# Performance work log

Hardware: AMD Instinct MI355X
Metric: run time of the kernel (lower is better)

Reference implementation:

```python
import jax, jax.numpy as jnp
import numpy as np

TEMPERATURE = 0.2
NUMBER_CLASSES = 1000
LOSS_SCALE = 0.001

N, F = 8192, 256
M = 20000
DEPTH = 4


def setup_inputs() -> dict:
    key = jax.random.key(0)
    k1, k2, k3, k4 = jax.random.split(key, 4)
    gt_labels = jax.random.randint(k1, (N,), 0, NUMBER_CLASSES, dtype=jnp.int32)
    box_features = jax.random.normal(k2, (N, F), dtype=jnp.float32)
    memory = jax.random.normal(k3, (M, F), dtype=jnp.float32)
    trace_idx = jax.random.randint(k4, (NUMBER_CLASSES, DEPTH), 0, M, dtype=jnp.int32)
    return {"gt_labels": gt_labels, "box_features": box_features,
            "memory": memory, "trace_idx": trace_idx}


def reference(gt_labels, box_features, memory, trace_idx):
    # logits[i, j] = dot(f_i, m_j) / T  (the nested python loops fused into one GEMM)
    logits = jnp.einsum('nf,mf->nm', box_features, memory) / TEMPERATURE  # [N, M]
    # fenmu = sum_j exp(logits)  ->  log(fenmu) = logsumexp
    lse = jax.nn.logsumexp(logits, axis=-1)  # [N]
    # gather the trace entries for each item's label: [N, DEPTH]
    traces = trace_idx[gt_labels]  # [N, DEPTH]
    sel = jnp.take_along_axis(logits, traces, axis=1)  # [N, DEPTH]
    depth_w = jnp.arange(DEPTH, dtype=logits.dtype)  # gj = depth
    sum_gj = depth_w.sum()  # sum of layer weights (0+1+2+3)
    # per item: -sum_d gj * log(sim_d / fenmu) / sum_gj
    per_item = -jnp.sum((sel - lse[:, None]) * depth_w, axis=-1) / sum_gj  # [N]
    # background filter: items with label == number_classes contribute nothing
    fg = (gt_labels != NUMBER_CLASSES)
    loss = jnp.sum(jnp.where(fg, per_item, 0.0)) * LOSS_SCALE
    return loss
```

## Files before the change

kernel.cpp:

```cpp
#include <hip/hip_runtime.h>
#include <hip/hip_bf16.h>
#include <stdint.h>

#define NROWS 8192
#define FDIM 256
#define MCOLS 20000
#define NT32 625
#define MSPLIT 16
#define NCLS 1000
#define LOG2E 1.44269504088896f
#define LN2   0.69314718055994f


typedef short short8 __attribute__((ext_vector_type(8)));
typedef float f32x16 __attribute__((ext_vector_type(16)));

typedef __attribute__((address_space(3))) unsigned int lds_u32;
typedef const __attribute__((address_space(1))) unsigned int glb_u32;

__device__ __forceinline__ float ex2(float x) {
    float r;
    asm("v_exp_f32 %0, %1" : "=v"(r) : "v"(x));
    return r;
}

__device__ __forceinline__ unsigned short f2bf(float x) {
    unsigned u = __float_as_uint(x);
    unsigned r = (u + 0x7FFFu + ((u >> 16) & 1u)) >> 16;
    return (unsigned short)r;
}

__device__ __forceinline__ float vmax16(f32x16 v) {
    float x0 = fmaxf(fmaxf(v[0],  v[1]),  v[2]);
    float x1 = fmaxf(fmaxf(v[3],  v[4]),  v[5]);
    float x2 = fmaxf(fmaxf(v[6],  v[7]),  v[8]);
    float x3 = fmaxf(fmaxf(v[9],  v[10]), v[11]);
    float x4 = fmaxf(fmaxf(v[12], v[13]), v[14]);
    float x5 = fmaxf(fmaxf(x0, x1), x2);
    float x6 = fmaxf(fmaxf(x3, x4), v[15]);
    return fmaxf(x5, x6);
}

__global__ void prep_kernel(const float* __restrict__ Mem, unsigned short* __restrict__ Mb2,
                            const float* __restrict__ F, unsigned short* __restrict__ Fb) {
    int b = blockIdx.x;
    if (b < 2500) {
        int g = b * 256 + threadIdx.x;
        int s = g & 63, kk = (g >> 6) & 15, t = g >> 10;
        const float* src = Mem + (size_t)(t * 32 + (s & 31)) * FDIM + kk * 16 + (s >> 5) * 8;
        float4 v0 = ((const float4*)src)[0];
        float4 v1 = ((const float4*)src)[1];
        short8 w;
        w[0] = (short)f2bf(v0.x); w[1] = (short)f2bf(v0.y);
        w[2] = (short)f2bf(v0.z); w[3] = (short)f2bf(v0.w);
        w[4] = (short)f2bf(v1.x); w[5] = (short)f2bf(v1.y);
        w[6] = (short)f2bf(v1.z); w[7] = (short)f2bf(v1.w);
        *(short8*)(Mb2 + (size_t)g * 8) = w;
    } else {
        int idx = (b - 2500) * 256 + threadIdx.x;
        float4 v = ((const float4*)F)[idx];
        const float sc = 5.0f * LOG2E;
        ushort4 o;
        o.x = f2bf(v.x * sc); o.y = f2bf(v.y * sc);
        o.z = f2bf(v.z * sc); o.w = f2bf(v.w * sc);
        ((ushort4*)Fb)[idx] = o;
    }
}

__global__ void sel_kernel(const int* __restrict__ gt, const float* __restrict__ F,
                           const float* __restrict__ Mem, const int* __restrict__ trace,
                           float* __restrict__ wsel) {
    int lane = threadIdx.x & 63, wid = threadIdx.x >> 6;
    int i = blockIdx.x * 4 + wid;
    int label = gt[i];
    float w = 0.0f;
    if (label >= 0 && label < NCLS) {
        float4 fv = ((const float4*)(F + (size_t)i * FDIM))[lane];
        #pragma unroll
        for (int d = 1; d <= 3; ++d) {
            int tr = trace[label * 4 + d];
            float4 mv = ((const float4*)(Mem + (size_t)tr * FDIM))[lane];
            float dot = fv.x*mv.x + fv.y*mv.y + fv.z*mv.z + fv.w*mv.w;
            #pragma unroll
            for (int off = 32; off >= 1; off >>= 1) dot += __shfl_xor(dot, off, 64);
            w += (float)d * dot;
        }
    }
    if (lane == 0) wsel[i] = w * 5.0f;
}

__global__ __launch_bounds__(256, 2) void lse_gemm(
        const unsigned short* __restrict__ Fb, const unsigned short* __restrict__ Mb2,
        float* __restrict__ pm, float* __restrict__ ps) {
    __shared__ __align__(16) char smem[2 * 32768];

    const int split  = blockIdx.x;
    const int rowblk = blockIdx.y;
    const int tid  = threadIdx.x;
    const int lane = tid & 63, wid = tid >> 6;
    const int r0 = lane & 31;
    const int hi = lane >> 5;
    const int rowbase = rowblk * 256 + wid * 64;
    const int l16 = lane << 4;

    short8 al[16], ah[16];
    #pragma unroll
    for (int kk = 0; kk < 16; ++kk) {
        al[kk] = *(const short8*)(Fb + (size_t)(rowbase + r0)      * FDIM + kk * 16 + hi * 8);
        ah[kk] = *(const short8*)(Fb + (size_t)(rowbase + 32 + r0) * FDIM + kk * 16 + hi * 8);
    }

    float m0 = -3.0e38f, s0 = 0.0f, m1 = -3.0e38f, s1 = 0.0f;

    const int t0 = (split * NT32) / MSPLIT;
    const int t1 = ((split + 1) * NT32) / MSPLIT;
    const int nt = t1 - t0, nmac = nt >> 1, tail = nt & 1;

#define STAGE2(BUF, t)                                                             \
    do {                                                                           \
        const char* srcT = (const char*)Mb2 + (size_t)(t) * 16384 + l16;           \
        _Pragma("unroll")                                                          \
        for (int c = 0; c < 8; ++c) {                                              \
            __builtin_amdgcn_global_load_lds(                                      \
                (glb_u32*)(srcT + (wid * 8 + c) * 1024),                           \
                (lds_u32*)(smem + (BUF) * 32768 + (wid * 8 + c) * 1024),           \
                16, 0, 0);                                                         \
        }                                                                          \
    } while (0)

#define STAGE1(BUF, t)                                                             \
    do {                                                                           \
        const char* srcT = (const char*)Mb2 + (size_t)(t) * 16384 + l16;           \
        _Pragma("unroll")                                                          \
        for (int c = 0; c < 4; ++c) {                                              \
            __builtin_amdgcn_global_load_lds(                                      \
                (glb_u32*)(srcT + (wid * 4 + c) * 1024),                           \
                (lds_u32*)(smem + (BUF) * 32768 + (wid * 4 + c) * 1024),           \
                16, 0, 0);                                                         \
        }                                                                          \
    } while (0)

#define SUB(BB)                                                                    \
    do {                                                                           \
        const char* bp = smem + (BB) + l16;                                        \
        f32x16 accL = {0,0,0,0,0,0,0,0,0,0,0,0,0,0,0,0};                           \
        f32x16 accH = {0,0,0,0,0,0,0,0,0,0,0,0,0,0,0,0};                           \
        __builtin_amdgcn_s_setprio(1);                                             \
        _Pragma("unroll")                                                          \
        for (int kk = 0; kk < 16; ++kk) {                                          \
            short8 b = *(const short8*)(bp + kk * 1024);                           \
            accL = __builtin_amdgcn_mfma_f32_32x32x16_bf16(b, al[kk], accL, 0, 0, 0); \
            accH = __builtin_amdgcn_mfma_f32_32x32x16_bf16(b, ah[kk], accH, 0, 0, 0); \
        }                                                                          \
        __builtin_amdgcn_s_setprio(0);                                             \
        {                                                                          \
            float nm = fmaxf(vmax16(accL), m0);                                    \
            float p0 = 0.f, p1 = 0.f, p2 = 0.f, p3 = 0.f;                          \
            _Pragma("unroll")                                                      \
            for (int i = 0; i < 16; i += 4) {                                      \
                p0 += ex2(accL[i]     - nm); p1 += ex2(accL[i + 1] - nm);          \
                p2 += ex2(accL[i + 2] - nm); p3 += ex2(accL[i + 3] - nm);          \
            }                                                                      \
            s0 = fmaf(s0, ex2(m0 - nm), (p0 + p1) + (p2 + p3));                    \
            m0 = nm;                                                               \
        }                                                                          \
        {                                                                          \
            float nm = fmaxf(vmax16(accH), m1);                                    \
            float p0 = 0.f, p1 = 0.f, p2 = 0.f, p3 = 0.f;                          \
            _Pragma("unroll")                                                      \
            for (int i = 0; i < 16; i += 4) {                                      \
                p0 += ex2(accH[i]     - nm); p1 += ex2(accH[i + 1] - nm);          \
                p2 += ex2(accH[i + 2] - nm); p3 += ex2(accH[i + 3] - nm);          \
            }                                                                      \
            s1 = fmaf(s1, ex2(m1 - nm), (p0 + p1) + (p2 + p3));                    \
            m1 = nm;                                                               \
        }                                                                          \
    } while (0)

    STAGE2(0, t0);
    __syncthreads();

    for (int mi = 0; mi < nmac; ++mi) {
        const int bb = (mi & 1) * 32768;
        if (mi + 1 < nmac)      STAGE2((mi & 1) ^ 1, t0 + 2 * mi + 2);
        else if (tail)          STAGE1((mi & 1) ^ 1, t0 + 2 * mi + 2);
        SUB(bb);
        SUB(bb + 16384);
        __syncthreads();
    }
    if (tail) SUB((nmac & 1) * 32768);

#undef SUB
#undef STAGE1
#undef STAGE2

    {
        float om = __shfl_xor(m0, 32, 64);
        float os = __shfl_xor(s0, 32, 64);
        float nm = fmaxf(m0, om);
        float sf = fmaf(s0, ex2(m0 - nm), os * ex2(om - nm));
        if (lane < 32) {
            pm[split * NROWS + rowbase + lane] = nm;
            ps[split * NROWS + rowbase + lane] = sf;
        }
    }
    {
        float om = __shfl_xor(m1, 32, 64);
        float os = __shfl_xor(s1, 32, 64);
        float nm = fmaxf(m1, om);
        float sf = fmaf(s1, ex2(m1 - nm), os * ex2(om - nm));
        if (lane < 32) {
            pm[split * NROWS + rowbase + 32 + lane] = nm;
            ps[split * NROWS + rowbase + 32 + lane] = sf;
        }
    }
}

__global__ void finalize_kernel(const int* __restrict__ gt, const float* __restrict__ wsel,
                                const float* __restrict__ pm, const float* __restrict__ ps,
                                float* __restrict__ bpart) {
    int tid = threadIdx.x;
    int i = blockIdx.x * 256 + tid;
    float mv[MSPLIT];
    float M = -3.0e38f;
    #pragma unroll
    for (int k = 0; k < MSPLIT; ++k) { mv[k] = pm[k * NROWS + i]; M = fmaxf(M, mv[k]); }
    float S = 0.0f;
    #pragma unroll
    for (int k = 0; k < MSPLIT; ++k) S += ps[k * NROWS + i] * ex2(mv[k] - M);
    float lse = (M + __log2f(S)) * LN2;
    int label = gt[i];
    float per = (label >= 0 && label < NCLS) ? (lse - wsel[i] * (1.0f / 6.0f)) : 0.0f;
    #pragma unroll
    for (int off = 32; off >= 1; off >>= 1) per += __shfl_xor(per, off, 64);
    __shared__ float red[4];
    int lane = tid & 63, wid = tid >> 6;
    if (lane == 0) red[wid] = per;
    __syncthreads();
    if (tid == 0) bpart[blockIdx.x] = red[0] + red[1] + red[2] + red[3];
}

__global__ void sum_kernel(const float* __restrict__ bpart, float* __restrict__ out) {
    int tid = threadIdx.x;
    float v = (tid < 32) ? bpart[tid] : 0.0f;
    #pragma unroll
    for (int off = 32; off >= 1; off >>= 1) v += __shfl_xor(v, off, 64);
    if (tid == 0) out[0] = 0.001f * v;
}

extern "C" void kernel_launch(void* const* d_in, const int* in_sizes, int n_in,
                              void* d_out, int out_size, void* d_ws, size_t ws_size,
                              hipStream_t stream) {
    const int*   gt    = (const int*)d_in[0];
    const float* F     = (const float*)d_in[1];
    const float* Mem   = (const float*)d_in[2];
    const int*   trace = (const int*)d_in[3];
    float* out = (float*)d_out;

    char* w = (char*)d_ws;
    unsigned short* Mb2 = (unsigned short*)w;
    unsigned short* Fb  = (unsigned short*)(w + 10240000);
    float* wsel  = (float*)(w + 14434304);
    float* pm    = (float*)(w + 14467072);
    float* ps    = (float*)(w + 14991360);
    float* bpart = (float*)(w + 15515648);

    prep_kernel<<<dim3(4548), dim3(256), 0, stream>>>(Mem, Mb2, F, Fb);
    sel_kernel<<<dim3(NROWS / 4), dim3(256), 0, stream>>>(gt, F, Mem, trace, wsel);
    lse_gemm<<<dim3(MSPLIT, NROWS / 256), dim3(256), 0, stream>>>(Fb, Mb2, pm, ps);
    finalize_kernel<<<dim3(NROWS / 256), dim3(256), 0, stream>>>(gt, wsel, pm, ps, bpart);
    sum_kernel<<<dim3(1), dim3(64), 0, stream>>>(bpart, out);
}
```

Measured before the change: 103.3 us.

## Software-pipeline MFMA with softmax of previous tile, fuse sel into prep, halve splits

```diff
diff --git a/kernel.cpp b/kernel.cpp
--- a/kernel.cpp
+++ b/kernel.cpp
@@ -6,7 +6,7 @@
 #define FDIM 256
 #define MCOLS 20000
 #define NT32 625
-#define MSPLIT 16
+#define MSPLIT 8
 #define NCLS 1000
 #define LOG2E 1.44269504088896f
 #define LN2   0.69314718055994f
@@ -42,7 +42,9 @@
 }
 
 __global__ void prep_kernel(const float* __restrict__ Mem, unsigned short* __restrict__ Mb2,
-                            const float* __restrict__ F, unsigned short* __restrict__ Fb) {
+                            const float* __restrict__ F, unsigned short* __restrict__ Fb,
+                            const int* __restrict__ gt, const int* __restrict__ trace,
+                            float* __restrict__ wsel) {
     int b = blockIdx.x;
     if (b < 2500) {
         int g = b * 256 + threadIdx.x;
@@ -56,7 +58,7 @@
         w[4] = (short)f2bf(v1.x); w[5] = (short)f2bf(v1.y);
         w[6] = (short)f2bf(v1.z); w[7] = (short)f2bf(v1.w);
         *(short8*)(Mb2 + (size_t)g * 8) = w;
-    } else {
+    } else if (b < 4548) {
         int idx = (b - 2500) * 256 + threadIdx.x;
         float4 v = ((const float4*)F)[idx];
         const float sc = 5.0f * LOG2E;
@@ -64,35 +66,32 @@
         o.x = f2bf(v.x * sc); o.y = f2bf(v.y * sc);
         o.z = f2bf(v.z * sc); o.w = f2bf(v.w * sc);
         ((ushort4*)Fb)[idx] = o;
-    }
-}
-
-__global__ void sel_kernel(const int* __restrict__ gt, const float* __restrict__ F,
-                           const float* __restrict__ Mem, const int* __restrict__ trace,
-                           float* __restrict__ wsel) {
-    int lane = threadIdx.x & 63, wid = threadIdx.x >> 6;
-    int i = blockIdx.x * 4 + wid;
-    int label = gt[i];
-    float w = 0.0f;
-    if (label >= 0 && label < NCLS) {
-        float4 fv = ((const float4*)(F + (size_t)i * FDIM))[lane];
-        #pragma unroll
-        for (int d = 1; d <= 3; ++d) {
-            int tr = trace[label * 4 + d];
-            float4 mv = ((const float4*)(Mem + (size_t)tr * FDIM))[lane];
-            float dot = fv.x*mv.x + fv.y*mv.y + fv.z*mv.z + fv.w*mv.w;
+    } else {
+        int lane = threadIdx.x & 63, wid = threadIdx.x >> 6;
+        int i = (b - 4548) * 4 + wid;
+        int label = gt[i];
+        float w = 0.0f;
+        if (label >= 0 && label < NCLS) {
+            float4 fv = ((const float4*)(F + (size_t)i * FDIM))[lane];
             #pragma unroll
-            for (int off = 32; off >= 1; off >>= 1) dot += __shfl_xor(dot, off, 64);
-            w += (float)d * dot;
+            for (int d = 1; d <= 3; ++d) {
+                int tr = trace[label * 4 + d];
+                float4 mv = ((const float4*)(Mem + (size_t)tr * FDIM))[lane];
+                float dot = fv.x*mv.x + fv.y*mv.y + fv.z*mv.z + fv.w*mv.w;
+                #pragma unroll
+                for (int off = 32; off >= 1; off >>= 1) dot += __shfl_xor(dot, off, 64);
+                w += (float)d * dot;
+            }
         }
-    }
-    if (lane == 0) wsel[i] = w * 5.0f;
-}
-
-__global__ __launch_bounds__(256, 2) void lse_gemm(
+        if (lane == 0) wsel[i] = w * 5.0f;
+    }
+}
+
+__global__ __attribute__((amdgpu_flat_work_group_size(256, 256), amdgpu_waves_per_eu(1, 1)))
+void lse_gemm(
         const unsigned short* __restrict__ Fb, const unsigned short* __restrict__ Mb2,
         float* __restrict__ pm, float* __restrict__ ps) {
-    __shared__ __align__(16) char smem[2 * 32768];
+    __shared__ __align__(16) char smem[2 * 16384];
 
     const int split  = blockIdx.x;
     const int rowblk = blockIdx.y;
@@ -111,88 +110,116 @@
     }
 
     float m0 = -3.0e38f, s0 = 0.0f, m1 = -3.0e38f, s1 = 0.0f;
+    float nmL, nmH, q0, q1, q2, q3, r0x, r1x, r2x, r3x;
+    f32x16 accLA, accHA, accLB, accHB;
 
     const int t0 = (split * NT32) / MSPLIT;
     const int t1 = ((split + 1) * NT32) / MSPLIT;
-    const int nt = t1 - t0, nmac = nt >> 1, tail = nt & 1;
-
-#define STAGE2(BUF, t)                                                             \
-    do {                                                                           \
-        const char* srcT = (const char*)Mb2 + (size_t)(t) * 16384 + l16;           \
-        _Pragma("unroll")                                                          \
-        for (int c = 0; c < 8; ++c) {                                              \
-            __builtin_amdgcn_global_load_lds(                                      \
-                (glb_u32*)(srcT + (wid * 8 + c) * 1024),                           \
-                (lds_u32*)(smem + (BUF) * 32768 + (wid * 8 + c) * 1024),           \
-                16, 0, 0);                                                         \
-        }                                                                          \
-    } while (0)
-
-#define STAGE1(BUF, t)                                                             \
+
+#define STAGE(BUF, t)                                                              \
     do {                                                                           \
         const char* srcT = (const char*)Mb2 + (size_t)(t) * 16384 + l16;           \
         _Pragma("unroll")                                                          \
         for (int c = 0; c < 4; ++c) {                                              \
             __builtin_amdgcn_global_load_lds(                                      \
                 (glb_u32*)(srcT + (wid * 4 + c) * 1024),                           \
-                (lds_u32*)(smem + (BUF) * 32768 + (wid * 4 + c) * 1024),           \
+                (lds_u32*)(smem + (BUF) * 16384 + (wid * 4 + c) * 1024),           \
                 16, 0, 0);                                                         \
         }                                                                          \
     } while (0)
 
-#define SUB(BB)                                                                    \
+#define MFMA_K(BP, CUR, KK)                                                        \
+    {                                                                              \
+        short8 b_ = *(const short8*)((BP) + (KK) * 1024);                          \
+        accL##CUR = __builtin_amdgcn_mfma_f32_32x32x16_bf16(b_, al[KK], accL##CUR, 0, 0, 0); \
+        accH##CUR = __builtin_amdgcn_mfma_f32_32x32x16_bf16(b_, ah[KK], accH##CUR, 0, 0, 0); \
+    }
+
+#define SM_P0(P)                                                                   \
+    nmL = fmaxf(vmax16(accL##P), m0); nmH = fmaxf(vmax16(accH##P), m1);            \
+    q0 = q1 = q2 = q3 = 0.f; r0x = r1x = r2x = r3x = 0.f;
+
+#define SM_P1(P)                                                                   \
+    q0 += ex2(accL##P[0] - nmL); q1 += ex2(accL##P[1] - nmL);                      \
+    q2 += ex2(accL##P[2] - nmL); q3 += ex2(accL##P[3] - nmL);                      \
+    q0 += ex2(accL##P[4] - nmL); q1 += ex2(accL##P[5] - nmL);                      \
+    q2 += ex2(accL##P[6] - nmL); q3 += ex2(accL##P[7] - nmL);
+
+#define SM_P2(P)                                                                   \
+    q0 += ex2(accL##P[8]  - nmL); q1 += ex2(accL##P[9]  - nmL);                    \
+    q2 += ex2(accL##P[10] - nmL); q3 += ex2(accL##P[11] - nmL);                    \
+    q0 += ex2(accL##P[12] - nmL); q1 += ex2(accL##P[13] - nmL);                    \
+    q2 += ex2(accL##P[14] - nmL); q3 += ex2(accL##P[15] - nmL);                    \
+    s0 = fmaf(s0, ex2(m0 - nmL), (q0 + q1) + (q2 + q3)); m0 = nmL;
+
+#define SM_P3(P)                                                                   \
+    r0x += ex2(accH##P[0]  - nmH); r1x += ex2(accH##P[1]  - nmH);                  \
+    r2x += ex2(accH##P[2]  - nmH); r3x += ex2(accH##P[3]  - nmH);                  \
+    r0x += ex2(accH##P[4]  - nmH); r1x += ex2(accH##P[5]  - nmH);                  \
+    r2x += ex2(accH##P[6]  - nmH); r3x += ex2(accH##P[7]  - nmH);                  \
+    r0x += ex2(accH##P[8]  - nmH); r1x += ex2(accH##P[9]  - nmH);                  \
+    r2x += ex2(accH##P[10] - nmH); r3x += ex2(accH##P[11] - nmH);                  \
+    r0x += ex2(accH##P[12] - nmH); r1x += ex2(accH##P[13] - nmH);                  \
+    r2x += ex2(accH##P[14] - nmH); r3x += ex2(accH##P[15] - nmH);                  \
+    s1 = fmaf(s1, ex2(m1 - nmH), (r0x + r1x) + (r2x + r3x)); m1 = nmH;
+
+#define PIPE(BUF, CUR, PRV)                                                        \
     do {                                                                           \
-        const char* bp = smem + (BB) + l16;                                        \
-        f32x16 accL = {0,0,0,0,0,0,0,0,0,0,0,0,0,0,0,0};                           \
-        f32x16 accH = {0,0,0,0,0,0,0,0,0,0,0,0,0,0,0,0};                           \
-        __builtin_amdgcn_s_setprio(1);                                             \
-        _Pragma("unroll")                                                          \
-        for (int kk = 0; kk < 16; ++kk) {                                          \
-            short8 b = *(const short8*)(bp + kk * 1024);                           \
-            accL = __builtin_amdgcn_mfma_f32_32x32x16_bf16(b, al[kk], accL, 0, 0, 0); \
-            accH = __builtin_amdgcn_mfma_f32_32x32x16_bf16(b, ah[kk], accH, 0, 0, 0); \
-        }                                                                          \
-        __builtin_amdgcn_s_setprio(0);                                             \
-        {                                                                          \
-            float nm = fmaxf(vmax16(accL), m0);                                    \
-            float p0 = 0.f, p1 = 0.f, p2 = 0.f, p3 = 0.f;                          \
-            _Pragma("unroll")                                                      \
-            for (int i = 0; i < 16; i += 4) {                                      \
-                p0 += ex2(accL[i]     - nm); p1 += ex2(accL[i + 1] - nm);          \
-                p2 += ex2(accL[i + 2] - nm); p3 += ex2(accL[i + 3] - nm);          \
-            }                                                                      \
-            s0 = fmaf(s0, ex2(m0 - nm), (p0 + p1) + (p2 + p3));                    \
-            m0 = nm;                                                               \
-        }                                                                          \
-        {                                                                          \
-            float nm = fmaxf(vmax16(accH), m1);                                    \
-            float p0 = 0.f, p1 = 0.f, p2 = 0.f, p3 = 0.f;                          \
-            _Pragma("unroll")                                                      \
-            for (int i = 0; i < 16; i += 4) {                                      \
-                p0 += ex2(accH[i]     - nm); p1 += ex2(accH[i + 1] - nm);          \
-                p2 += ex2(accH[i + 2] - nm); p3 += ex2(accH[i + 3] - nm);          \
-            }                                                                      \
-            s1 = fmaf(s1, ex2(m1 - nm), (p0 + p1) + (p2 + p3));                    \
-            m1 = nm;                                                               \
-        }                                                                          \
+        const char* bp_ = smem + (BUF) * 16384 + l16;                              \
+        f32x16 z_ = {0,0,0,0,0,0,0,0,0,0,0,0,0,0,0,0};                             \
+        accL##CUR = z_; accH##CUR = z_;                                            \
+        _Pragma("unroll") for (int kk = 0;  kk < 4;  ++kk) MFMA_K(bp_, CUR, kk)    \
+        SM_P0(PRV)                                                                 \
+        _Pragma("unroll") for (int kk = 4;  kk < 8;  ++kk) MFMA_K(bp_, CUR, kk)    \
+        SM_P1(PRV)                                                                 \
+        _Pragma("unroll") for (int kk = 8;  kk < 12; ++kk) MFMA_K(bp_, CUR, kk)    \
+        SM_P2(PRV)                                                                 \
+        _Pragma("unroll") for (int kk = 12; kk < 16; ++kk) MFMA_K(bp_, CUR, kk)    \
+        SM_P3(PRV)                                                                 \
     } while (0)
 
-    STAGE2(0, t0);
+#define MFMA_ONLY(BUF, CUR)                                                        \
+    do {                                                                           \
+        const char* bp_ = smem + (BUF) * 16384 + l16;                              \
+        f32x16 z_ = {0,0,0,0,0,0,0,0,0,0,0,0,0,0,0,0};                             \
+        accL##CUR = z_; accH##CUR = z_;                                            \
+        _Pragma("unroll") for (int kk = 0; kk < 16; ++kk) MFMA_K(bp_, CUR, kk)     \
+    } while (0)
+
+#define SM_FULL(P) do { SM_P0(P) SM_P1(P) SM_P2(P) SM_P3(P) } while (0)
+
+    STAGE(0, t0);
     __syncthreads();
-
-    for (int mi = 0; mi < nmac; ++mi) {
-        const int bb = (mi & 1) * 32768;
-        if (mi + 1 < nmac)      STAGE2((mi & 1) ^ 1, t0 + 2 * mi + 2);
-        else if (tail)          STAGE1((mi & 1) ^ 1, t0 + 2 * mi + 2);
-        SUB(bb);
-        SUB(bb + 16384);
+    STAGE(1, t0 + 1);
+    MFMA_ONLY(0, A);
+    __syncthreads();
+
+    int t = t0 + 1;
+    while (t + 2 <= t1) {
+        STAGE(0, t + 1);
+        PIPE(1, B, A);
         __syncthreads();
-    }
-    if (tail) SUB((nmac & 1) * 32768);
-
-#undef SUB
-#undef STAGE1
-#undef STAGE2
+        if (t + 2 < t1) STAGE(1, t + 2);
+        PIPE(0, A, B);
+        __syncthreads();
+        t += 2;
+    }
+    if (t < t1) {
+        PIPE(1, B, A);
+        SM_FULL(B);
+    } else {
+        SM_FULL(A);
+    }
+
+#undef SM_FULL
+#undef MFMA_ONLY
+#undef PIPE
+#undef SM_P3
+#undef SM_P2
+#undef SM_P1
+#undef SM_P0
+#undef MFMA_K
+#undef STAGE
 
     {
         float om = __shfl_xor(m0, 32, 64);
@@ -265,8 +292,7 @@
     float* ps    = (float*)(w + 14991360);
     float* bpart = (float*)(w + 15515648);
 
-    prep_kernel<<<dim3(4548), dim3(256), 0, stream>>>(Mem, Mb2, F, Fb);
-    sel_kernel<<<dim3(NROWS / 4), dim3(256), 0, stream>>>(gt, F, Mem, trace, wsel);
+    prep_kernel<<<dim3(6596), dim3(256), 0, stream>>>(Mem, Mb2, F, Fb, gt, trace, wsel);
     lse_gemm<<<dim3(MSPLIT, NROWS / 256), dim3(256), 0, stream>>>(Fb, Mb2, pm, ps);
     finalize_kernel<<<dim3(NROWS / 256), dim3(256), 0, stream>>>(gt, wsel, pm, ps, bpart);
     sum_kernel<<<dim3(1), dim3(64), 0, stream>>>(bpart, out);
```

Measured after the change: 98.68 us. 4.5% less time.
